# Kernel tuning notes

Measured on AMD Instinct MI355X. Metric: run time of the kernel, lower is better.

## Reference

```python
import jax, jax.numpy as jnp
import numpy as np

TOP_K = 5
TEMPERATURE = 0.1
EPS = 1e-12


def _normalize(x):
    # F.normalize(x, dim=-1): x / max(||x||, eps)
    n = jnp.linalg.norm(x, axis=-1, keepdims=True)
    return x / jnp.maximum(n, EPS)


def setup_inputs() -> dict:
    key = jax.random.key(0)
    k1, k2, k3 = jax.random.split(key, 3)
    B, N, D = 1024, 200000, 128
    query = jax.random.normal(k1, (B, D), dtype=jnp.float32)
    # memory bank stores L2-normalized keys (MemoryBank.build applies F.normalize)
    memory = _normalize(jax.random.normal(k2, (N, D), dtype=jnp.float32))
    index_map = jnp.arange(N, dtype=jnp.int64)
    exclude_indices = jax.random.randint(k3, (B,), 0, N, dtype=jnp.int64)
    return {"query": query, "memory": memory, "index_map": index_map,
            "exclude_indices": exclude_indices}


def reference(query, memory, index_map, exclude_indices):
    # cosine similarity: normalize query, memory is already normalized
    qn = _normalize(query)                       # [B, D]
    sim = qn @ memory.T                          # [B, N]
    # exclude own training sample (training-time self-exclusion)
    mask = exclude_indices[:, None] == index_map[None, :]   # [B, N]
    sim = jnp.where(mask, -jnp.inf, sim)
    # top-k (effective_top_k = min(top_k, N-1) = TOP_K here)
    top_sim, top_idx = jax.lax.top_k(sim, TOP_K)             # [B, K]
    weights = jax.nn.softmax(top_sim / TEMPERATURE, axis=-1)  # [B, K]
    vecs = memory[top_idx]                                   # [B, K, D]
    retrieved = jnp.einsum('bk,bkd->bd', weights, vecs)      # weighted sum
    retrieved = _normalize(retrieved)
    distances = 1.0 - top_sim[:, 0]                          # [B]
    return retrieved, distances, weights
```

## Files before the change

kernel.cpp:

```cpp
#include <hip/hip_runtime.h>
#include <hip/hip_bf16.h>
#include <math.h>

#define D128 128
#define TOPK 5
#define NP 200704
#define NCH2 12544
#define NSTRIP 392
#define MARGIN 0.008f
#define CAP 1024
#define SCAP 96

typedef __attribute__((ext_vector_type(8))) short short8;
typedef __attribute__((ext_vector_type(4))) float f32x4;

__device__ __forceinline__ short f2bf(float f) {
    union { float f; unsigned u; } c; c.f = f;
    unsigned u = c.u + 0x7FFFu + ((c.u >> 16) & 1u);
    return (short)(u >> 16);
}

__device__ __forceinline__ unsigned pkbf(float x, float y) {
    __hip_bfloat162 h = __float22bfloat162_rn(make_float2(x, y));
    unsigned u; __builtin_memcpy(&u, &h, 4);
    return u;
}

template <int NN>
__device__ __forceinline__ void insertg(float (&v)[NN], int (&x)[NN], float nv, int nj) {
    bool g[NN];
    #pragma unroll
    for (int i = 0; i < NN; ++i) g[i] = nv > v[i];
    #pragma unroll
    for (int i = NN - 1; i > 0; --i) {
        v[i] = g[i - 1] ? v[i - 1] : (g[i] ? nv : v[i]);
        x[i] = g[i - 1] ? x[i - 1] : (g[i] ? nj : x[i]);
    }
    v[0] = g[0] ? nv : v[0];
    x[0] = g[0] ? nj : x[0];
}
template <int NN>
__device__ __forceinline__ void insertv(float (&v)[NN], float nv) {
    bool g[NN];
    #pragma unroll
    for (int i = 0; i < NN; ++i) g[i] = nv > v[i];
    #pragma unroll
    for (int i = NN - 1; i > 0; --i)
        v[i] = g[i - 1] ? v[i - 1] : (g[i] ? nv : v[i]);
    v[0] = g[0] ? nv : v[0];
}

__global__ void qnorm_kernel(const float* __restrict__ q, float* __restrict__ qn,
                             short* __restrict__ qbf) {
    int b = blockIdx.x, t = threadIdx.x;
    float v0 = q[(size_t)b * D128 + t];
    float v1 = q[(size_t)b * D128 + t + 64];
    float ss = v0 * v0 + v1 * v1;
    #pragma unroll
    for (int off = 32; off > 0; off >>= 1) ss += __shfl_xor(ss, off, 64);
    float scale = 1.0f / fmaxf(sqrtf(ss), 1e-12f);
    float a0 = v0 * scale, a1 = v1 * scale;
    qn[(size_t)b * D128 + t] = a0;
    qn[(size_t)b * D128 + t + 64] = a1;
    qbf[(size_t)b * D128 + t] = f2bf(a0);
    qbf[(size_t)b * D128 + t + 64] = f2bf(a1);
}

#define MFMA16(a, b, c) __builtin_amdgcn_mfma_f32_16x16x32_bf16(a, b, c, 0, 0, 0)

__global__ __launch_bounds__(256, 3) void simtopk_max(
    const short* __restrict__ qbf, const float* __restrict__ mem,
    _Float16* __restrict__ candT, _Float16* __restrict__ stripT, int N) {
    __shared__ short sK[64 * 136];
    __shared__ _Float16 sC[256 * 40];
    const int strip = blockIdx.x;
    const int qsg = blockIdx.y;
    const int t = threadIdx.x, w = t >> 6, lane = t & 63;
    const int n = lane & 15, quad = lane >> 4;
    const int qbase = qsg * 256 + w * 64;

    short8 bq[4][4];
    #pragma unroll
    for (int f = 0; f < 4; ++f) {
        const short* qrow = qbf + (size_t)(qbase + f * 16 + n) * D128 + quad * 8;
        #pragma unroll
        for (int s = 0; s < 4; ++s) bq[f][s] = *(const short8*)(qrow + s * 32);
    }

    const size_t k0 = (size_t)strip * 512;
    const int srow = t >> 4, scol = t & 15;
    const float* gbase = mem + (k0 + srow) * (size_t)D128 + scol * 8;
    const bool tail = (k0 + 512 > (size_t)N);

    float4 fa[8];

    auto loadg = [&](int g) {
        const float* base = gbase + (size_t)g * 64 * D128;
        #pragma unroll
        for (int i = 0; i < 4; ++i) {
            const float4* p = (const float4*)(base + (size_t)i * 16 * D128);
            if (tail) {
                size_t key = k0 + (size_t)(g * 64 + srow + i * 16);
                if (key >= (size_t)N) p = (const float4*)mem;
            }
            fa[2 * i]     = p[0];
            fa[2 * i + 1] = p[1];
        }
    };
    auto storesk = [&](int g) {
        #pragma unroll
        for (int i = 0; i < 4; ++i) {
            uint4 wv;
            wv.x = pkbf(fa[2 * i].x,     fa[2 * i].y);
            wv.y = pkbf(fa[2 * i].z,     fa[2 * i].w);
            wv.z = pkbf(fa[2 * i + 1].x, fa[2 * i + 1].y);
            wv.w = pkbf(fa[2 * i + 1].z, fa[2 * i + 1].w);
            if (tail && (k0 + (size_t)(g * 64 + srow + i * 16) >= (size_t)N))
                wv = make_uint4(0, 0, 0, 0);
            *((uint4*)&sK[(srow + 16 * i) * 136 + scol * 8]) = wv;
        }
    };

    loadg(0);
    storesk(0);
    __syncthreads();
    loadg(1);

    for (int round = 0; round < 8; ++round) {
        #pragma unroll
        for (int tt = 0; tt < 4; ++tt) {
            const short* ab = &sK[(tt * 16 + n) * 136 + quad * 8];
            short8 a0 = *(const short8*)(ab);
            short8 a1 = *(const short8*)(ab + 32);
            short8 a2 = *(const short8*)(ab + 64);
            short8 a3 = *(const short8*)(ab + 96);
            f32x4 c0 = {0.f, 0.f, 0.f, 0.f}, c1 = c0, c2 = c0, c3 = c0;
            c0 = MFMA16(a0, bq[0][0], c0);
            c1 = MFMA16(a0, bq[1][0], c1);
            c2 = MFMA16(a0, bq[2][0], c2);
            c3 = MFMA16(a0, bq[3][0], c3);
            c0 = MFMA16(a1, bq[0][1], c0);
            c1 = MFMA16(a1, bq[1][1], c1);
            c2 = MFMA16(a1, bq[2][1], c2);
            c3 = MFMA16(a1, bq[3][1], c3);
            c0 = MFMA16(a2, bq[0][2], c0);
            c1 = MFMA16(a2, bq[1][2], c1);
            c2 = MFMA16(a2, bq[2][2], c2);
            c3 = MFMA16(a2, bq[3][2], c3);
            c0 = MFMA16(a3, bq[0][3], c0);
            c1 = MFMA16(a3, bq[1][3], c1);
            c2 = MFMA16(a3, bq[2][3], c2);
            c3 = MFMA16(a3, bq[3][3], c3);
            float m0 = fmaxf(fmaxf(c0[0], c0[1]), fmaxf(c0[2], c0[3]));
            float m1 = fmaxf(fmaxf(c1[0], c1[1]), fmaxf(c1[2], c1[3]));
            float m2 = fmaxf(fmaxf(c2[0], c2[1]), fmaxf(c2[2], c2[3]));
            float m3 = fmaxf(fmaxf(c3[0], c3[1]), fmaxf(c3[2], c3[3]));
            m0 = fmaxf(m0, __shfl_xor(m0, 16, 64)); m0 = fmaxf(m0, __shfl_xor(m0, 32, 64));
            m1 = fmaxf(m1, __shfl_xor(m1, 16, 64)); m1 = fmaxf(m1, __shfl_xor(m1, 32, 64));
            m2 = fmaxf(m2, __shfl_xor(m2, 16, 64)); m2 = fmaxf(m2, __shfl_xor(m2, 32, 64));
            m3 = fmaxf(m3, __shfl_xor(m3, 16, 64)); m3 = fmaxf(m3, __shfl_xor(m3, 32, 64));
            float msel = (quad == 0) ? m0 : (quad == 1) ? m1 : (quad == 2) ? m2 : m3;
            sC[(w * 64 + quad * 16 + n) * 40 + round * 4 + tt] = (_Float16)msel;
        }
        if (round < 7) {
            __syncthreads();
            storesk(round + 1);
            __syncthreads();
            if (round < 6) loadg(round + 2);
        }
    }

    __syncthreads();
    {
        int q = qsg * 256 + t;
        short* dst = (short*)candT + (size_t)q * NCH2 + strip * 32;
        float mx = -3e38f;
        #pragma unroll
        for (int j = 0; j < 4; ++j) {
            short8 v = *(const short8*)(&sC[t * 40 + j * 8]);
            *(short8*)(dst + j * 8) = v;
            #pragma unroll
            for (int e = 0; e < 8; ++e) {
                short sv = v[e]; _Float16 hv; __builtin_memcpy(&hv, &sv, 2);
                mx = fmaxf(mx, (float)hv);
            }
        }
        stripT[(size_t)q * NSTRIP + strip] = (_Float16)mx;
    }
}

__global__ __launch_bounds__(256, 4) void finalize_batch(
    const _Float16* __restrict__ candT, const _Float16* __restrict__ stripT,
    const float* __restrict__ mem, const float* __restrict__ qn,
    const int* __restrict__ index_map, const int* __restrict__ excl,
    float* __restrict__ outR, float* __restrict__ outD, float* __restrict__ outW, int N) {
    const int q = blockIdx.x, t = threadIdx.x;
    const int w = t >> 6, lane = t & 63;

    __shared__ __align__(16) float sQ[D128];
    __shared__ __align__(16) _Float16 sS[NSTRIP];
    __shared__ unsigned short sStr[SCAP];
    __shared__ unsigned short sList[CAP];
    __shared__ int sScnt, sSov, sCnt, sOv;
    __shared__ float sThr;
    __shared__ float sMrg[4 * 6];
    __shared__ float sWv[4 * TOPK];
    __shared__ int   sWk[4 * TOPK];
    __shared__ float sW[TOPK];
    __shared__ int   sJ[TOPK];

    if (t < 128) sQ[t] = qn[(size_t)q * D128 + t];
    if (t == 0) { sScnt = 0; sSov = 0; sCnt = 0; sOv = 0; }
    if (t < NSTRIP / 8)
        *(short8*)(&sS[t * 8]) =
            *(const short8*)((const short*)stripT + (size_t)q * NSTRIP + t * 8);
    __syncthreads();

    float pv[6];
    #pragma unroll
    for (int i = 0; i < 6; ++i) pv[i] = -3e38f;
    for (int i = t; i < NSTRIP; i += 256) {
        float v = (float)sS[i];
        if (v > pv[5]) insertv<6>(pv, v);
    }
    #pragma unroll
    for (int r = 0; r < 6; ++r) {
        float bv = pv[0];
        #pragma unroll
        for (int off = 32; off > 0; off >>= 1) bv = fmaxf(bv, __shfl_xor(bv, off, 64));
        int ml = (pv[0] == bv) ? lane : 64;
        #pragma unroll
        for (int off = 32; off > 0; off >>= 1) ml = min(ml, __shfl_xor(ml, off, 64));
        if (lane == ml) {
            #pragma unroll
            for (int i = 0; i < 5; ++i) pv[i] = pv[i + 1];
            pv[5] = -3e38f;
        }
        if (lane == 0) sMrg[w * 6 + r] = bv;
    }
    __syncthreads();
    if (t == 0) {
        float b6[6];
        #pragma unroll
        for (int i = 0; i < 6; ++i) b6[i] = -3e38f;
        for (int j = 0; j < 24; ++j) {
            float v = sMrg[j];
            if (v > b6[5]) insertv<6>(b6, v);
        }
        sThr = b6[5] - 2.0f * MARGIN;
    }
    __syncthreads();

    const float thr = sThr;
    for (int i = t; i < NSTRIP; i += 256) {
        if ((float)sS[i] >= thr) {
            int p = atomicAdd(&sScnt, 1);
            if (p < SCAP) sStr[p] = (unsigned short)i; else sSov = 1;
        }
    }
    __syncthreads();
    const int scnt = min(sScnt, SCAP);

    if (!sSov) {
        for (int base = 0; base < scnt; base += 8) {
            int si = base + (t >> 5);
            if (si < scnt) {
                int ch = (int)sStr[si] * 32 + (t & 31);
                float v = (float)candT[(size_t)q * NCH2 + ch];
                if (v >= thr) {
                    int p = atomicAdd(&sCnt, 1);
                    if (p < CAP) sList[p] = (unsigned short)ch; else sOv = 1;
                }
            }
        }
    }
    __syncthreads();
    const int ov = (sSov || sOv) ? 1 : 0;
    const int cnt = ov ? NCH2 : min(sCnt, CAP);

    const int exq = excl[q];
    float tv[TOPK]; int ti[TOPK];
    #pragma unroll
    for (int i = 0; i < TOPK; ++i) { tv[i] = -3e38f; ti[i] = -1; }
    const int rounds = (cnt + 15) >> 4;
    for (int r = 0; r < rounds; ++r) {
        int slot = r * 16 + (t >> 4);
        int ch = (slot < cnt) ? (ov ? slot : (int)sList[slot]) : -1;
        int key = ch * 16 + (t & 15);
        float v = -3e38f;
        if (ch >= 0 && key < N && index_map[key] != exq) {
            const float4* mr = (const float4*)(mem + (size_t)key * D128);
            const float4* qv = (const float4*)sQ;
            float acc = 0.f;
            #pragma unroll
            for (int d = 0; d < 32; ++d) {
                float4 a = mr[d], b = qv[d];
                acc += a.x * b.x + a.y * b.y + a.z * b.z + a.w * b.w;
            }
            v = acc;
        }
        if (v > tv[TOPK - 1]) insertg<TOPK>(tv, ti, v, key);
    }

    #pragma unroll
    for (int r = 0; r < TOPK; ++r) {
        float bv = tv[0]; int bk = ti[0];
        #pragma unroll
        for (int off = 32; off > 0; off >>= 1) {
            float ovv = __shfl_xor(bv, off, 64);
            int   okk = __shfl_xor(bk, off, 64);
            if (ovv > bv || (ovv == bv && (unsigned)okk < (unsigned)bk)) { bv = ovv; bk = okk; }
        }
        if (tv[0] == bv && ti[0] == bk) {
            #pragma unroll
            for (int i = 0; i < TOPK - 1; ++i) { tv[i] = tv[i + 1]; ti[i] = ti[i + 1]; }
            tv[TOPK - 1] = -3e38f; ti[TOPK - 1] = -1;
        }
        if (lane == 0) { sWv[w * TOPK + r] = bv; sWk[w * TOPK + r] = bk; }
    }
    __syncthreads();
    if (t == 0) {
        float bv[TOPK]; int bi[TOPK];
        #pragma unroll
        for (int i = 0; i < TOPK; ++i) { bv[i] = -3e38f; bi[i] = -1; }
        for (int j = 0; j < 4 * TOPK; ++j) {
            float v = sWv[j];
            if (v > bv[TOPK - 1]) insertg<TOPK>(bv, bi, v, sWk[j]);
        }
        float m = bv[0], ex[TOPK], sum = 0.f;
        #pragma unroll
        for (int k = 0; k < TOPK; ++k) { ex[k] = __expf((bv[k] - m) * 10.0f); sum += ex[k]; }
        float inv = 1.0f / sum;
        #pragma unroll
        for (int k = 0; k < TOPK; ++k) {
            float wk = ex[k] * inv;
            sW[k] = wk; sJ[k] = bi[k];
            outW[(size_t)q * TOPK + k] = wk;
        }
        outD[q] = 1.0f - bv[0];
    }
    __syncthreads();
    if (t < 64) {
        float r0 = 0.f, r1 = 0.f;
        #pragma unroll
        for (int k = 0; k < TOPK; ++k) {
            const float* mr = mem + (size_t)sJ[k] * D128;
            r0 += sW[k] * mr[t];
            r1 += sW[k] * mr[t + 64];
        }
        float ss = r0 * r0 + r1 * r1;
        #pragma unroll
        for (int off = 32; off > 0; off >>= 1) ss += __shfl_xor(ss, off, 64);
        float scale = 1.0f / fmaxf(sqrtf(ss), 1e-12f);
        outR[(size_t)q * D128 + t]      = r0 * scale;
        outR[(size_t)q * D128 + t + 64] = r1 * scale;
    }
}

extern "C" void kernel_launch(void* const* d_in, const int* in_sizes, int n_in,
                              void* d_out, int out_size, void* d_ws, size_t ws_size,
                              hipStream_t stream) {
    const float* query  = (const float*)d_in[0];
    const float* memory = (const float*)d_in[1];
    const int* index_map = (const int*)d_in[2];
    const int* excl      = (const int*)d_in[3];

    const int B = in_sizes[3];
    const int N = in_sizes[2];

    char* ws = (char*)d_ws;
    float*    qn     = (float*)(ws);
    short*    qbf    = (short*)(ws + 524288);
    _Float16* candT  = (_Float16*)(ws + 786432);
    _Float16* stripT = (_Float16*)(ws + 786432 + 25690112);

    float* outR = (float*)d_out;
    float* outD = outR + (size_t)B * D128;
    float* outW = outD + B;

    qnorm_kernel<<<B, 64, 0, stream>>>(query, qn, qbf);
    dim3 gridC(NSTRIP, 4);
    simtopk_max<<<gridC, 256, 0, stream>>>(qbf, memory, candT, stripT, N);
    finalize_batch<<<B, 256, 0, stream>>>(candT, stripT, memory, qn, index_map, excl,
                                          outR, outD, outW, N);
}
```

Measured before the change: 259.6 us.

## Swizzle grid for L2 reuse, cut shuffles, pad LDS stride, raise occupancy

The 2D grid becomes a 1D grid whose block index is remapped so that the four query groups for each group of 8 strips run close together, letting memory-bank tiles be reused from cache. The cross-quad max reduction switches to a butterfly exchange of selected values, which needs 3 shuffles instead of 8. The sC row stride changes from 40 to 44 to cut LDS bank conflicts, and the readback is split into two 8-byte loads because the new stride breaks 16-byte alignment. Launch bounds go from 3 to 4 blocks per SIMD, which could force register spilling.

```diff
diff --git a/kernel.cpp b/kernel.cpp
--- a/kernel.cpp
+++ b/kernel.cpp
@@ -10,8 +10,10 @@
 #define MARGIN 0.008f
 #define CAP 1024
 #define SCAP 96
+#define SCST 44
 
 typedef __attribute__((ext_vector_type(8))) short short8;
+typedef __attribute__((ext_vector_type(4))) short s4v;
 typedef __attribute__((ext_vector_type(4))) float f32x4;
 
 __device__ __forceinline__ short f2bf(float f) {
@@ -68,15 +70,17 @@
 
 #define MFMA16(a, b, c) __builtin_amdgcn_mfma_f32_16x16x32_bf16(a, b, c, 0, 0, 0)
 
-__global__ __launch_bounds__(256, 3) void simtopk_max(
+__global__ __launch_bounds__(256, 4) void simtopk_max(
     const short* __restrict__ qbf, const float* __restrict__ mem,
     _Float16* __restrict__ candT, _Float16* __restrict__ stripT, int N) {
     __shared__ short sK[64 * 136];
-    __shared__ _Float16 sC[256 * 40];
-    const int strip = blockIdx.x;
-    const int qsg = blockIdx.y;
+    __shared__ _Float16 sC[256 * SCST];
+    const int b = blockIdx.x;
+    const int strip = (b & 7) + ((b >> 5) << 3);
+    const int qsg = (b >> 3) & 3;
     const int t = threadIdx.x, w = t >> 6, lane = t & 63;
     const int n = lane & 15, quad = lane >> 4;
+    const bool qb0 = (quad & 1) != 0, qb1 = (quad & 2) != 0;
     const int qbase = qsg * 256 + w * 64;
 
     short8 bq[4][4];
@@ -155,12 +159,14 @@
             float m1 = fmaxf(fmaxf(c1[0], c1[1]), fmaxf(c1[2], c1[3]));
             float m2 = fmaxf(fmaxf(c2[0], c2[1]), fmaxf(c2[2], c2[3]));
             float m3 = fmaxf(fmaxf(c3[0], c3[1]), fmaxf(c3[2], c3[3]));
-            m0 = fmaxf(m0, __shfl_xor(m0, 16, 64)); m0 = fmaxf(m0, __shfl_xor(m0, 32, 64));
-            m1 = fmaxf(m1, __shfl_xor(m1, 16, 64)); m1 = fmaxf(m1, __shfl_xor(m1, 32, 64));
-            m2 = fmaxf(m2, __shfl_xor(m2, 16, 64)); m2 = fmaxf(m2, __shfl_xor(m2, 32, 64));
-            m3 = fmaxf(m3, __shfl_xor(m3, 16, 64)); m3 = fmaxf(m3, __shfl_xor(m3, 32, 64));
-            float msel = (quad == 0) ? m0 : (quad == 1) ? m1 : (quad == 2) ? m2 : m3;
-            sC[(w * 64 + quad * 16 + n) * 40 + round * 4 + tt] = (_Float16)msel;
+            float u0 = qb0 ? m1 : m0, u1 = qb0 ? m0 : m1;
+            float u2 = qb0 ? m3 : m2, u3 = qb0 ? m2 : m3;
+            float v0 = qb1 ? u2 : u0, v1 = qb1 ? u3 : u1;
+            float v2 = qb1 ? u0 : u2, v3 = qb1 ? u1 : u3;
+            float A = fmaxf(v0, __shfl_xor(v2, 32, 64));
+            float B = fmaxf(v1, __shfl_xor(v3, 32, 64));
+            float fin = fmaxf(A, __shfl_xor(B, 16, 64));
+            sC[(w * 64 + quad * 16 + n) * SCST + round * 4 + tt] = (_Float16)fin;
         }
         if (round < 7) {
             __syncthreads();
@@ -177,7 +183,11 @@
         float mx = -3e38f;
         #pragma unroll
         for (int j = 0; j < 4; ++j) {
-            short8 v = *(const short8*)(&sC[t * 40 + j * 8]);
+            s4v lo = *(const s4v*)(&sC[t * SCST + j * 8]);
+            s4v hi = *(const s4v*)(&sC[t * SCST + j * 8 + 4]);
+            short8 v;
+            v[0] = lo[0]; v[1] = lo[1]; v[2] = lo[2]; v[3] = lo[3];
+            v[4] = hi[0]; v[5] = hi[1]; v[6] = hi[2]; v[7] = hi[3];
             *(short8*)(dst + j * 8) = v;
             #pragma unroll
             for (int e = 0; e < 8; ++e) {
@@ -379,8 +389,7 @@
     float* outW = outD + B;
 
     qnorm_kernel<<<B, 64, 0, stream>>>(query, qn, qbf);
-    dim3 gridC(NSTRIP, 4);
-    simtopk_max<<<gridC, 256, 0, stream>>>(qbf, memory, candT, stripT, N);
+    simtopk_max<<<NSTRIP * 4, 256, 0, stream>>>(qbf, memory, candT, stripT, N);
     finalize_batch<<<B, 256, 0, stream>>>(candT, stripT, memory, qn, index_map, excl,
                                           outR, outD, outW, N);
 }
```

Result: slower. 413.0 us (+59.1%).
